# Optimization experiments

Hardware: AMD Instinct MI355X
Metric: run time of the kernel (lower is better)

## Reference

```python
import jax, jax.numpy as jnp
import numpy as np

B, N, F = 512, 2048, 64
T = 4            # number of atom types
H1, H2 = 64, 32  # hidden widths; final layer outputs 1 (per-atom energy)


def setup_inputs() -> dict:
    key = jax.random.key(0)
    ks = jax.random.split(key, 8)
    x = jax.random.normal(ks[0], (B, N, F), dtype=jnp.float32)
    atomic_numbers = jax.random.randint(ks[1], (N,), 0, T)
    s = 0.05
    # Per-type MLP parameters, stacked over the type axis (torch Linear layout: [out, in]).
    w0 = jax.random.normal(ks[2], (T, H1, F), dtype=jnp.float32) * s
    b0 = jax.random.normal(ks[3], (T, H1), dtype=jnp.float32) * s
    w1 = jax.random.normal(ks[4], (T, H2, H1), dtype=jnp.float32) * s
    b1 = jax.random.normal(ks[5], (T, H2), dtype=jnp.float32) * s
    w2 = jax.random.normal(ks[6], (T, 1, H2), dtype=jnp.float32) * s
    b2 = jax.random.normal(ks[7], (T, 1), dtype=jnp.float32) * s
    return {"x": x, "atomic_numbers": atomic_numbers,
            "w0": w0, "b0": b0, "w1": w1, "b1": b1, "w2": w2, "b2": b2}


def reference(x, atomic_numbers, w0, b0, w1, b1, w2, b2):
    # Behler-Parrinello: route each atom through the MLP of its atom type,
    # then sum per-atom energies over atoms.  The torch version gathers atoms
    # by type, runs each type's MLP, and scatters back; here we evaluate all
    # T type-MLPs batched over the type axis and select with a one-hot mask
    # (identical math, jit-friendly, no data-dependent shapes).
    onehot = jax.nn.one_hot(atomic_numbers, w0.shape[0], dtype=x.dtype)  # [N, T]
    h = jax.nn.silu(jnp.einsum('bnf,thf->tbnh', x, w0) + b0[:, None, None, :])   # [T,B,N,H1]
    h = jax.nn.silu(jnp.einsum('tbnh,tgh->tbng', h, w1) + b1[:, None, None, :])  # [T,B,N,H2]
    e = jnp.einsum('tbng,tog->tbno', h, w2) + b2[:, None, None, :]               # [T,B,N,1]
    e = e[..., 0]                                                                # [T,B,N]
    per_atom = jnp.einsum('tbn,nt->bn', e, onehot)  # select the matching type per atom
    return per_atom.sum(axis=-1)                    # [B]
```

## Files before the change

kernel.cpp:

```cpp
#include <hip/hip_runtime.h>
#include <hip/hip_bf16.h>


#define B_ 512
#define N_ 2048
#define F_ 64
#define T_ 4
#define H1_ 64
#define H2_ 32

#define BT 16
#define WAVES 4
#define NPW 32
#define NCHUNK (WAVES * NPW)

typedef __attribute__((ext_vector_type(8))) short bf16x8;
typedef __attribute__((ext_vector_type(4))) short bf16x4;
typedef __attribute__((ext_vector_type(4))) float f32x4;

__device__ inline float silu_f(float v) {
    return v * __builtin_amdgcn_rcpf(1.0f + __expf(-v));
}

__device__ inline bf16x8 pack8(float4 a, float4 b) {
    union { __hip_bfloat162 h[4]; bf16x8 v; } u;
    u.h[0] = __float22bfloat162_rn({a.x, a.y});
    u.h[1] = __float22bfloat162_rn({a.z, a.w});
    u.h[2] = __float22bfloat162_rn({b.x, b.y});
    u.h[3] = __float22bfloat162_rn({b.z, b.w});
    return u.v;
}

__device__ inline bf16x4 pack4(float a, float b, float c, float d) {
    union { __hip_bfloat162 h[2]; bf16x4 v; } u;
    u.h[0] = __float22bfloat162_rn({a, b});
    u.h[1] = __float22bfloat162_rn({c, d});
    return u.v;
}

__global__ __launch_bounds__(256, 2) void bpnn_kernel(
    const float* __restrict__ x, const int* __restrict__ an,
    const float* __restrict__ w0, const float* __restrict__ b0,
    const float* __restrict__ w1, const float* __restrict__ b1,
    const float* __restrict__ w2, const float* __restrict__ b2,
    float* __restrict__ out)
{
    __shared__ __align__(16) __hip_bfloat16 w0s[T_][H1_][72];
    __shared__ __align__(16) __hip_bfloat16 w1s[T_][H2_][72];
    __shared__ __align__(16) __hip_bfloat16 trb[WAVES][BT][72];
    __shared__ __align__(16) __hip_bfloat16 w2s[T_][H2_];
    __shared__ __align__(16) __hip_bfloat16 b0s[T_][H1_];
    __shared__ __align__(16) __hip_bfloat16 b1s[T_][H2_];

    const int tid = threadIdx.x;

    for (int i = tid; i < T_ * H1_ * F_; i += 256)
        w0s[i >> 12][(i >> 6) & 63][i & 63] = __float2bfloat16(w0[i]);
    for (int i = tid; i < T_ * H2_ * H1_; i += 256)
        w1s[i >> 11][(i >> 6) & 31][i & 63] = __float2bfloat16(w1[i]);
    if (tid < T_ * H2_) w2s[tid >> 5][tid & 31] = __float2bfloat16(w2[tid]);
    if (tid < T_ * H1_) b0s[tid >> 6][tid & 63] = __float2bfloat16(b0[tid]);
    if (tid < T_ * H2_) b1s[tid >> 5][tid & 31] = __float2bfloat16(b1[tid]);
    const float b2r0 = b2[0], b2r1 = b2[1], b2r2 = b2[2], b2r3 = b2[3];
    __syncthreads();

    const int wave = tid >> 6;
    const int lane = tid & 63;
    const int lr   = lane & 15;
    const int q    = lane >> 4;
    const int b0i  = blockIdx.y * BT;
    const int gn0  = blockIdx.x * NCHUNK + wave * NPW;

    const float4* xp = reinterpret_cast<const float4*>(
        x + (size_t)(b0i + lr) * N_ * F_ + (size_t)gn0 * F_ + q * 8);

    __hip_bfloat16* trbw = &trb[wave][lr][0];

    float esum = 0.f;
    float bsum = 0.f;

    float4 pa = xp[0], pb = xp[1], pc = xp[8], pd = xp[9];
    int tpre = an[gn0];

    for (int it = 0; it < NPW; ++it) {
        const int t = __builtin_amdgcn_readfirstlane(tpre);
        float4 xa = pa, xb = pb, xc = pc, xd = pd;

        {
            const int nx = (it + 1 < NPW) ? (it + 1) : (NPW - 1);
            const int o = nx * 16;
            pa = xp[o]; pb = xp[o + 1]; pc = xp[o + 8]; pd = xp[o + 9];
            tpre = an[gn0 + nx];
        }

        bf16x8 xb0 = pack8(xa, xb);
        bf16x8 xb1 = pack8(xc, xd);

        const __hip_bfloat16* w0t = &w0s[t][0][0];
        const __hip_bfloat16* w1t = &w1s[t][0][0];
        const int rowoff = lr * 72 + q * 8;

        f32x4 acc[4] = {{0,0,0,0},{0,0,0,0},{0,0,0,0},{0,0,0,0}};
#pragma unroll
        for (int nt = 0; nt < 4; ++nt) {
            bf16x8 aw0 = *reinterpret_cast<const bf16x8*>(w0t + nt * 16 * 72 + rowoff);
            acc[nt] = __builtin_amdgcn_mfma_f32_16x16x32_bf16(aw0, xb0, acc[nt], 0, 0, 0);
            bf16x8 aw1 = *reinterpret_cast<const bf16x8*>(w0t + nt * 16 * 72 + rowoff + 32);
            acc[nt] = __builtin_amdgcn_mfma_f32_16x16x32_bf16(aw1, xb1, acc[nt], 0, 0, 0);
        }
#pragma unroll
        for (int nt = 0; nt < 4; ++nt) {
            bf16x4 bb = *reinterpret_cast<const bf16x4*>(&b0s[t][nt * 16 + q * 4]);
            float v0 = silu_f(acc[nt][0] + __bfloat162float(((__hip_bfloat16*)&bb)[0]));
            float v1 = silu_f(acc[nt][1] + __bfloat162float(((__hip_bfloat16*)&bb)[1]));
            float v2 = silu_f(acc[nt][2] + __bfloat162float(((__hip_bfloat16*)&bb)[2]));
            float v3 = silu_f(acc[nt][3] + __bfloat162float(((__hip_bfloat16*)&bb)[3]));
            *reinterpret_cast<bf16x4*>(trbw + nt * 16 + q * 4) = pack4(v0, v1, v2, v3);
        }
        __builtin_amdgcn_wave_barrier();

        bf16x8 hb0 = *reinterpret_cast<const bf16x8*>(trbw + q * 8);
        bf16x8 hb1 = *reinterpret_cast<const bf16x8*>(trbw + 32 + q * 8);
        __builtin_amdgcn_wave_barrier();

        f32x4 accB[2] = {{0,0,0,0},{0,0,0,0}};
#pragma unroll
        for (int mt = 0; mt < 2; ++mt) {
            bf16x8 aw0 = *reinterpret_cast<const bf16x8*>(w1t + mt * 16 * 72 + rowoff);
            accB[mt] = __builtin_amdgcn_mfma_f32_16x16x32_bf16(aw0, hb0, accB[mt], 0, 0, 0);
            bf16x8 aw1 = *reinterpret_cast<const bf16x8*>(w1t + mt * 16 * 72 + rowoff + 32);
            accB[mt] = __builtin_amdgcn_mfma_f32_16x16x32_bf16(aw1, hb1, accB[mt], 0, 0, 0);
        }
#pragma unroll
        for (int mt = 0; mt < 2; ++mt) {
            bf16x4 bb = *reinterpret_cast<const bf16x4*>(&b1s[t][mt * 16 + q * 4]);
            bf16x4 ww = *reinterpret_cast<const bf16x4*>(&w2s[t][mt * 16 + q * 4]);
#pragma unroll
            for (int r = 0; r < 4; ++r) {
                float v = silu_f(accB[mt][r] + __bfloat162float(((__hip_bfloat16*)&bb)[r]));
                esum += v * __bfloat162float(((__hip_bfloat16*)&ww)[r]);
            }
        }
        bsum += (t == 0) ? b2r0 : (t == 1) ? b2r1 : (t == 2) ? b2r2 : b2r3;
    }

    esum += __shfl_xor(esum, 16);
    esum += __shfl_xor(esum, 32);

    __syncthreads();
    float* red = reinterpret_cast<float*>(&w0s[0][0][0]);
    if (tid < BT) red[tid] = 0.0f;
    __syncthreads();
    if (q == 0) atomicAdd(&red[lr], esum + bsum);
    __syncthreads();
    if (tid < BT) atomicAdd(&out[b0i + tid], red[tid]);
}

extern "C" void kernel_launch(void* const* d_in, const int* in_sizes, int n_in,
                              void* d_out, int out_size, void* d_ws, size_t ws_size,
                              hipStream_t stream) {
    const float* x  = (const float*)d_in[0];
    const int*   an = (const int*)d_in[1];
    const float* w0 = (const float*)d_in[2];
    const float* b0 = (const float*)d_in[3];
    const float* w1 = (const float*)d_in[4];
    const float* b1 = (const float*)d_in[5];
    const float* w2 = (const float*)d_in[6];
    const float* b2 = (const float*)d_in[7];
    float* out = (float*)d_out;

    hipMemsetAsync(out, 0, B_ * sizeof(float), stream);
    dim3 grid(N_ / NCHUNK, B_ / BT);
    bpnn_kernel<<<grid, 256, 0, stream>>>(x, an, w0, b0, w1, b1, w2, b2, out);
}
```

Before: 395.5 us.

## Assign one atom type per wave with register-resident weights and type bucketing

Each wave now processes only the atoms of one type within a 128-atom chunk. The chunk's atoms are bucketed by type with an in-block counting sort in shared memory. The type's weights and biases are loaded once into registers, which removes the per-block staging of weights into LDS and the per-iteration LDS weight reads. The b2 bias is added as count times b2 per wave. Risks are load imbalance across waves when type counts differ, indirect gathered x loads, and higher register pressure, now paired with a larger launch-bounds occupancy target.

New measurement: 383.0 us, median of 2. 1.03x faster.

```diff
diff --git a/kernel.cpp b/kernel.cpp
--- a/kernel.cpp
+++ b/kernel.cpp
@@ -11,8 +11,7 @@
 
 #define BT 16
 #define WAVES 4
-#define NPW 32
-#define NCHUNK (WAVES * NPW)
+#define NCHUNK 128
 
 typedef __attribute__((ext_vector_type(8))) short bf16x8;
 typedef __attribute__((ext_vector_type(4))) short bf16x4;
@@ -38,120 +37,143 @@
     return u.v;
 }
 
-__global__ __launch_bounds__(256, 2) void bpnn_kernel(
+__device__ inline float bf_at(bf16x4 v, int r) {
+    union { bf16x4 v; __hip_bfloat16 h[4]; } u; u.v = v;
+    return __bfloat162float(u.h[r]);
+}
+
+__global__ __launch_bounds__(256, 3) void bpnn_kernel(
     const float* __restrict__ x, const int* __restrict__ an,
     const float* __restrict__ w0, const float* __restrict__ b0,
     const float* __restrict__ w1, const float* __restrict__ b1,
     const float* __restrict__ w2, const float* __restrict__ b2,
     float* __restrict__ out)
 {
-    __shared__ __align__(16) __hip_bfloat16 w0s[T_][H1_][72];
-    __shared__ __align__(16) __hip_bfloat16 w1s[T_][H2_][72];
-    __shared__ __align__(16) __hip_bfloat16 trb[WAVES][BT][72];
-    __shared__ __align__(16) __hip_bfloat16 w2s[T_][H2_];
-    __shared__ __align__(16) __hip_bfloat16 b0s[T_][H1_];
-    __shared__ __align__(16) __hip_bfloat16 b1s[T_][H2_];
+    __shared__ __align__(16) __hip_bfloat16 trb[WAVES][BT][68];
+    __shared__ int sidx[NCHUNK];
+    __shared__ int cnt[T_], offs[T_], pos[T_];
+    __shared__ float red[BT];
 
-    const int tid = threadIdx.x;
-
-    for (int i = tid; i < T_ * H1_ * F_; i += 256)
-        w0s[i >> 12][(i >> 6) & 63][i & 63] = __float2bfloat16(w0[i]);
-    for (int i = tid; i < T_ * H2_ * H1_; i += 256)
-        w1s[i >> 11][(i >> 6) & 31][i & 63] = __float2bfloat16(w1[i]);
-    if (tid < T_ * H2_) w2s[tid >> 5][tid & 31] = __float2bfloat16(w2[tid]);
-    if (tid < T_ * H1_) b0s[tid >> 6][tid & 63] = __float2bfloat16(b0[tid]);
-    if (tid < T_ * H2_) b1s[tid >> 5][tid & 31] = __float2bfloat16(b1[tid]);
-    const float b2r0 = b2[0], b2r1 = b2[1], b2r2 = b2[2], b2r3 = b2[3];
-    __syncthreads();
-
+    const int tid  = threadIdx.x;
     const int wave = tid >> 6;
     const int lane = tid & 63;
     const int lr   = lane & 15;
     const int q    = lane >> 4;
     const int b0i  = blockIdx.y * BT;
-    const int gn0  = blockIdx.x * NCHUNK + wave * NPW;
+    const int n0   = blockIdx.x * NCHUNK;
+    const int t    = wave;
 
-    const float4* xp = reinterpret_cast<const float4*>(
-        x + (size_t)(b0i + lr) * N_ * F_ + (size_t)gn0 * F_ + q * 8);
+    const float* w0t = w0 + t * (H1_ * F_);
+    const float* w1t = w1 + t * (H2_ * H1_);
+    bf16x8 aw0[4][2], aw1[2][2];
+#pragma unroll
+    for (int nt = 0; nt < 4; ++nt)
+#pragma unroll
+        for (int kh = 0; kh < 2; ++kh) {
+            const float4* p = reinterpret_cast<const float4*>(
+                w0t + (nt * 16 + lr) * F_ + kh * 32 + q * 8);
+            aw0[nt][kh] = pack8(p[0], p[1]);
+        }
+#pragma unroll
+    for (int mt = 0; mt < 2; ++mt)
+#pragma unroll
+        for (int kh = 0; kh < 2; ++kh) {
+            const float4* p = reinterpret_cast<const float4*>(
+                w1t + (mt * 16 + lr) * H1_ + kh * 32 + q * 8);
+            aw1[mt][kh] = pack8(p[0], p[1]);
+        }
+    bf16x4 b0f[4], b1f[2], w2f[2];
+#pragma unroll
+    for (int nt = 0; nt < 4; ++nt) {
+        float4 v = *reinterpret_cast<const float4*>(b0 + t * H1_ + nt * 16 + q * 4);
+        b0f[nt] = pack4(v.x, v.y, v.z, v.w);
+    }
+#pragma unroll
+    for (int mt = 0; mt < 2; ++mt) {
+        float4 v = *reinterpret_cast<const float4*>(b1 + t * H2_ + mt * 16 + q * 4);
+        b1f[mt] = pack4(v.x, v.y, v.z, v.w);
+        float4 u = *reinterpret_cast<const float4*>(w2 + t * H2_ + mt * 16 + q * 4);
+        w2f[mt] = pack4(u.x, u.y, u.z, u.w);
+    }
+    const float b2t = b2[t];
 
+    if (tid < T_)  cnt[tid] = 0;
+    if (tid < BT)  red[tid] = 0.0f;
+    __syncthreads();
+    int myt = 0;
+    if (tid < NCHUNK) { myt = an[n0 + tid]; atomicAdd(&cnt[myt], 1); }
+    __syncthreads();
+    if (tid == 0) {
+        int o = 0;
+        for (int k = 0; k < T_; ++k) { offs[k] = o; pos[k] = o; o += cnt[k]; }
+    }
+    __syncthreads();
+    if (tid < NCHUNK) { int p = atomicAdd(&pos[myt], 1); sidx[p] = tid; }
+    __syncthreads();
+
+    const int beg = offs[t];
+    const int num = __builtin_amdgcn_readfirstlane(cnt[t]);
+
+    const float* xb_ = x + (size_t)(b0i + lr) * (N_ * F_) + (size_t)n0 * F_ + q * 8;
     __hip_bfloat16* trbw = &trb[wave][lr][0];
 
     float esum = 0.f;
-    float bsum = 0.f;
 
-    float4 pa = xp[0], pb = xp[1], pc = xp[8], pd = xp[9];
-    int tpre = an[gn0];
+    if (num > 0) {
+        int nl = sidx[beg];
+        const float4* p0 = reinterpret_cast<const float4*>(xb_ + nl * F_);
+        float4 pa = p0[0], pb = p0[1], pc = p0[8], pd = p0[9];
 
-    for (int it = 0; it < NPW; ++it) {
-        const int t = __builtin_amdgcn_readfirstlane(tpre);
-        float4 xa = pa, xb = pb, xc = pc, xd = pd;
+        for (int it = 0; it < num; ++it) {
+            bf16x8 xf0 = pack8(pa, pb);
+            bf16x8 xf1 = pack8(pc, pd);
+            {
+                int ii = (it + 1 < num) ? (it + 1) : it;
+                int nn = sidx[beg + ii];
+                const float4* pn = reinterpret_cast<const float4*>(xb_ + nn * F_);
+                pa = pn[0]; pb = pn[1]; pc = pn[8]; pd = pn[9];
+            }
 
-        {
-            const int nx = (it + 1 < NPW) ? (it + 1) : (NPW - 1);
-            const int o = nx * 16;
-            pa = xp[o]; pb = xp[o + 1]; pc = xp[o + 8]; pd = xp[o + 9];
-            tpre = an[gn0 + nx];
-        }
+            f32x4 acc[4] = {{0,0,0,0},{0,0,0,0},{0,0,0,0},{0,0,0,0}};
+#pragma unroll
+            for (int nt = 0; nt < 4; ++nt) {
+                acc[nt] = __builtin_amdgcn_mfma_f32_16x16x32_bf16(aw0[nt][0], xf0, acc[nt], 0, 0, 0);
+                acc[nt] = __builtin_amdgcn_mfma_f32_16x16x32_bf16(aw0[nt][1], xf1, acc[nt], 0, 0, 0);
+            }
+#pragma unroll
+            for (int nt = 0; nt < 4; ++nt) {
+                float v0 = silu_f(acc[nt][0] + bf_at(b0f[nt], 0));
+                float v1 = silu_f(acc[nt][1] + bf_at(b0f[nt], 1));
+                float v2 = silu_f(acc[nt][2] + bf_at(b0f[nt], 2));
+                float v3 = silu_f(acc[nt][3] + bf_at(b0f[nt], 3));
+                *reinterpret_cast<bf16x4*>(trbw + nt * 16 + q * 4) = pack4(v0, v1, v2, v3);
+            }
+            __builtin_amdgcn_wave_barrier();
 
-        bf16x8 xb0 = pack8(xa, xb);
-        bf16x8 xb1 = pack8(xc, xd);
+            bf16x8 hb0 = *reinterpret_cast<const bf16x8*>(trbw + q * 8);
+            bf16x8 hb1 = *reinterpret_cast<const bf16x8*>(trbw + 32 + q * 8);
+            __builtin_amdgcn_wave_barrier();
 
-        const __hip_bfloat16* w0t = &w0s[t][0][0];
-        const __hip_bfloat16* w1t = &w1s[t][0][0];
-        const int rowoff = lr * 72 + q * 8;
-
-        f32x4 acc[4] = {{0,0,0,0},{0,0,0,0},{0,0,0,0},{0,0,0,0}};
+            f32x4 accB[2] = {{0,0,0,0},{0,0,0,0}};
 #pragma unroll
-        for (int nt = 0; nt < 4; ++nt) {
-            bf16x8 aw0 = *reinterpret_cast<const bf16x8*>(w0t + nt * 16 * 72 + rowoff);
-            acc[nt] = __builtin_amdgcn_mfma_f32_16x16x32_bf16(aw0, xb0, acc[nt], 0, 0, 0);
-            bf16x8 aw1 = *reinterpret_cast<const bf16x8*>(w0t + nt * 16 * 72 + rowoff + 32);
-            acc[nt] = __builtin_amdgcn_mfma_f32_16x16x32_bf16(aw1, xb1, acc[nt], 0, 0, 0);
-        }
+            for (int mt = 0; mt < 2; ++mt) {
+                accB[mt] = __builtin_amdgcn_mfma_f32_16x16x32_bf16(aw1[mt][0], hb0, accB[mt], 0, 0, 0);
+                accB[mt] = __builtin_amdgcn_mfma_f32_16x16x32_bf16(aw1[mt][1], hb1, accB[mt], 0, 0, 0);
+            }
 #pragma unroll
-        for (int nt = 0; nt < 4; ++nt) {
-            bf16x4 bb = *reinterpret_cast<const bf16x4*>(&b0s[t][nt * 16 + q * 4]);
-            float v0 = silu_f(acc[nt][0] + __bfloat162float(((__hip_bfloat16*)&bb)[0]));
-            float v1 = silu_f(acc[nt][1] + __bfloat162float(((__hip_bfloat16*)&bb)[1]));
-            float v2 = silu_f(acc[nt][2] + __bfloat162float(((__hip_bfloat16*)&bb)[2]));
-            float v3 = silu_f(acc[nt][3] + __bfloat162float(((__hip_bfloat16*)&bb)[3]));
-            *reinterpret_cast<bf16x4*>(trbw + nt * 16 + q * 4) = pack4(v0, v1, v2, v3);
-        }
-        __builtin_amdgcn_wave_barrier();
-
-        bf16x8 hb0 = *reinterpret_cast<const bf16x8*>(trbw + q * 8);
-        bf16x8 hb1 = *reinterpret_cast<const bf16x8*>(trbw + 32 + q * 8);
-        __builtin_amdgcn_wave_barrier();
-
-        f32x4 accB[2] = {{0,0,0,0},{0,0,0,0}};
+            for (int mt = 0; mt < 2; ++mt) {
 #pragma unroll
-        for (int mt = 0; mt < 2; ++mt) {
-            bf16x8 aw0 = *reinterpret_cast<const bf16x8*>(w1t + mt * 16 * 72 + rowoff);
-            accB[mt] = __builtin_amdgcn_mfma_f32_16x16x32_bf16(aw0, hb0, accB[mt], 0, 0, 0);
-            bf16x8 aw1 = *reinterpret_cast<const bf16x8*>(w1t + mt * 16 * 72 + rowoff + 32);
-            accB[mt] = __builtin_amdgcn_mfma_f32_16x16x32_bf16(aw1, hb1, accB[mt], 0, 0, 0);
-        }
-#pragma unroll
-        for (int mt = 0; mt < 2; ++mt) {
-            bf16x4 bb = *reinterpret_cast<const bf16x4*>(&b1s[t][mt * 16 + q * 4]);
-            bf16x4 ww = *reinterpret_cast<const bf16x4*>(&w2s[t][mt * 16 + q * 4]);
-#pragma unroll
-            for (int r = 0; r < 4; ++r) {
-                float v = silu_f(accB[mt][r] + __bfloat162float(((__hip_bfloat16*)&bb)[r]));
-                esum += v * __bfloat162float(((__hip_bfloat16*)&ww)[r]);
+                for (int r = 0; r < 4; ++r) {
+                    float v = silu_f(accB[mt][r] + bf_at(b1f[mt], r));
+                    esum += v * bf_at(w2f[mt], r);
+                }
             }
         }
-        bsum += (t == 0) ? b2r0 : (t == 1) ? b2r1 : (t == 2) ? b2r2 : b2r3;
     }
 
     esum += __shfl_xor(esum, 16);
     esum += __shfl_xor(esum, 32);
-
-    __syncthreads();
-    float* red = reinterpret_cast<float*>(&w0s[0][0][0]);
-    if (tid < BT) red[tid] = 0.0f;
-    __syncthreads();
-    if (q == 0) atomicAdd(&red[lr], esum + bsum);
+    if (q == 0) atomicAdd(&red[lr], esum + (float)num * b2t);
     __syncthreads();
     if (tid < BT) atomicAdd(&out[b0i + tid], red[tid]);
 }
```
